# Kernel tuning notes

Measured on AMD Instinct MI355X. Metric: run time of the kernel, lower is better.

The kernel has to match this reference:

```python
import jax, jax.numpy as jnp
import numpy as np

N_NODES = 50000
N_EDGES = 1600000
D_IN = 128
D_E = 64
D_MID = 64
D_CAT = 2 * D_IN + D_E  # 320, input width of first Linear


def setup_inputs() -> dict:
    key = jax.random.key(0)
    ks = jax.random.split(key, 8)
    emb = jax.random.normal(ks[0], (N_NODES, D_IN), dtype=jnp.float32)
    src_idx = jax.random.randint(ks[1], (N_EDGES,), 0, N_NODES, dtype=jnp.int32)
    dst_idx = jax.random.randint(ks[2], (N_EDGES,), 0, N_NODES, dtype=jnp.int32)
    edge_feats = jax.random.normal(ks[3], (N_EDGES, D_E), dtype=jnp.float32)
    # nn.Linear default init: U(-1/sqrt(fan_in), 1/sqrt(fan_in))
    s1 = 1.0 / np.sqrt(D_CAT)
    s2 = 1.0 / np.sqrt(D_MID)
    W1 = jax.random.uniform(ks[4], (D_CAT, D_MID), jnp.float32, -s1, s1)
    b1 = jax.random.uniform(ks[5], (D_MID,), jnp.float32, -s1, s1)
    W2 = jax.random.uniform(ks[6], (D_MID, 1), jnp.float32, -s2, s2)
    b2 = jax.random.uniform(ks[7], (1,), jnp.float32, -s2, s2)
    return {"emb": emb, "src_idx": src_idx, "dst_idx": dst_idx,
            "edge_feats": edge_feats, "W1": W1, "b1": b1, "W2": W2, "b2": b2}


def reference(emb, src_idx, dst_idx, edge_feats, W1, b1, W2, b2):
    # Equivalent to concat([emb[i], emb[j], e_ij]) @ W1, but split so the
    # node-side projections are done once per node, then gathered per edge.
    W1_src = W1[:D_IN]            # [D_IN, D_MID]
    W1_dst = W1[D_IN:2 * D_IN]    # [D_IN, D_MID]
    W1_e = W1[2 * D_IN:]          # [D_E, D_MID]
    proj_src = emb @ W1_src       # [N, D_MID]
    proj_dst = emb @ W1_dst       # [N, D_MID]
    h = proj_src[src_idx] + proj_dst[dst_idx] + edge_feats @ W1_e + b1  # [E, D_MID]
    h = jax.nn.relu(h)
    logits = h @ W2[:, 0] + b2[0]  # [E]
    return logits
```

## Files before the change

kernel.cpp:

```cpp
#include <hip/hip_runtime.h>
#include <hip/hip_bf16.h>
#include <cstddef>

#define D_IN 128
#define D_E 64
#define D_MID 64

typedef __attribute__((ext_vector_type(8))) short bf16x8;
typedef __attribute__((ext_vector_type(4))) float f32x4;
typedef __attribute__((ext_vector_type(4))) int i32x4;

__device__ __forceinline__ short bf16_rne(float f) {
    __hip_bfloat16 h = __float2bfloat16(f);
    union { __hip_bfloat16 h; short s; } u; u.h = h;
    return u.s;
}

__device__ __forceinline__ void split2(float f, short& hi, short& lo) {
    unsigned u  = __float_as_uint(f);
    unsigned uh = u & 0xffff0000u;
    hi = (short)(uh >> 16);
    lo = bf16_rne(f - __uint_as_float(uh));
}

__global__ __launch_bounds__(128) void proj_kernel(
    const float* __restrict__ emb, const float* __restrict__ W1,
    const float* __restrict__ b1, float* __restrict__ P)
{
    const int j  = threadIdx.x;
    const int nb = blockIdx.x * 16;
    const float* Wbase = (j < 64) ? (W1 + j) : (W1 + 128 * 64 + (j - 64));

    float acc[16];
    #pragma unroll
    for (int i = 0; i < 16; ++i) acc[i] = 0.f;

    for (int kc = 0; kc < 8; ++kc) {
        float w[16];
        #pragma unroll
        for (int kk = 0; kk < 16; ++kk) w[kk] = Wbase[(kc * 16 + kk) * 64];
        #pragma unroll
        for (int i = 0; i < 16; ++i) {
            const float* e = emb + (size_t)(nb + i) * 128 + kc * 16;
            #pragma unroll
            for (int kk = 0; kk < 16; ++kk)
                acc[i] = fmaf(e[kk], w[kk], acc[i]);
        }
    }
    const float bias = (j < 64) ? b1[j] : 0.f;
    #pragma unroll
    for (int i = 0; i < 16; ++i)
        P[(size_t)(nb + i) * 128 + j] = acc[i] + bias;
}

__global__ __launch_bounds__(256) void edge_kernel(
    const float* __restrict__ ef,  const int* __restrict__ src,
    const int* __restrict__ dst,   const float* __restrict__ P,
    const float* __restrict__ W1,  const float* __restrict__ W2,
    const float* __restrict__ b2p, float* __restrict__ out)
{
    const int lane = threadIdx.x & 63;
    const int lr   = lane & 15;
    const int lg   = lane >> 4;
    const int wid  = threadIdx.x >> 6;
    const int wave = blockIdx.x * 4 + wid;
    const int ebase0 = wave * 128;

    const float* We = W1 + 256 * 64;
    bf16x8 bhi[2][4], blo[2][4];
    #pragma unroll
    for (int ks = 0; ks < 2; ++ks)
        #pragma unroll
        for (int nt = 0; nt < 4; ++nt) {
            #pragma unroll
            for (int i = 0; i < 8; ++i) {
                int kl = (i < 4) ? (lg * 4 + i) : (16 + lg * 4 + (i - 4));
                float f = We[(ks * 32 + kl) * 64 + nt * 16 + lr];
                short h, l; split2(f, h, l);
                bhi[ks][nt][i] = h; blo[ks][nt][i] = l;
            }
        }

    float w2v[4];
    #pragma unroll
    for (int nt = 0; nt < 4; ++nt) w2v[nt] = W2[nt * 16 + lr];
    const float b2 = b2p[0];

    i32x4 s4 = __builtin_nontemporal_load((const i32x4*)(src + ebase0 + lg * 4));
    i32x4 d4 = __builtin_nontemporal_load((const i32x4*)(dst + ebase0 + lg * 4));

    for (int t = 0; t < 8; ++t) {
        const int eb = ebase0 + t * 16;

        i32x4 s4n, d4n;
        if (t < 7) {
            s4n = __builtin_nontemporal_load((const i32x4*)(src + eb + 16 + lg * 4));
            d4n = __builtin_nontemporal_load((const i32x4*)(dst + eb + 16 + lg * 4));
        }

        f32x4 acc[4];
        #pragma unroll
        for (int nt = 0; nt < 4; ++nt) acc[nt] = (f32x4){0.f, 0.f, 0.f, 0.f};

        #pragma unroll
        for (int ks = 0; ks < 2; ++ks) {
            const float* abase = ef + (size_t)(eb + lr) * 64 + ks * 32 + lg * 4;
            f32x4 a0 = __builtin_nontemporal_load((const f32x4*)(abase));
            f32x4 a1 = __builtin_nontemporal_load((const f32x4*)(abase + 16));
            bf16x8 ahi, alo;
            #pragma unroll
            for (int i = 0; i < 4; ++i) {
                short h, l;
                split2(a0[i], h, l); ahi[i]     = h; alo[i]     = l;
                split2(a1[i], h, l); ahi[i + 4] = h; alo[i + 4] = l;
            }
            #pragma unroll
            for (int nt = 0; nt < 4; ++nt) {
                acc[nt] = __builtin_amdgcn_mfma_f32_16x16x32_bf16(ahi, bhi[ks][nt], acc[nt], 0, 0, 0);
                acc[nt] = __builtin_amdgcn_mfma_f32_16x16x32_bf16(ahi, blo[ks][nt], acc[nt], 0, 0, 0);
                acc[nt] = __builtin_amdgcn_mfma_f32_16x16x32_bf16(alo, bhi[ks][nt], acc[nt], 0, 0, 0);
            }
        }

        #pragma unroll
        for (int r = 0; r < 4; ++r) {
            const float* Ps = P + (size_t)s4[r] * 128 + lr;
            const float* Pd = P + (size_t)d4[r] * 128 + 64 + lr;
            float tot = 0.f;
            #pragma unroll
            for (int nt = 0; nt < 4; ++nt) {
                float h = acc[nt][r] + Ps[nt * 16] + Pd[nt * 16];
                h = fmaxf(h, 0.f);
                tot = fmaf(h, w2v[nt], tot);
            }
            tot += __shfl_xor(tot, 1);
            tot += __shfl_xor(tot, 2);
            tot += __shfl_xor(tot, 4);
            tot += __shfl_xor(tot, 8);
            if (lr == 0)
                __builtin_nontemporal_store(tot + b2, out + eb + lg * 4 + r);
        }

        s4 = s4n; d4 = d4n;
    }
}

extern "C" void kernel_launch(void* const* d_in, const int* in_sizes, int n_in,
                              void* d_out, int out_size, void* d_ws, size_t ws_size,
                              hipStream_t stream) {
    const float* emb = (const float*)d_in[0];
    const int*   src = (const int*)  d_in[1];
    const int*   dst = (const int*)  d_in[2];
    const float* ef  = (const float*)d_in[3];
    const float* W1  = (const float*)d_in[4];
    const float* b1  = (const float*)d_in[5];
    const float* W2  = (const float*)d_in[6];
    const float* b2  = (const float*)d_in[7];
    float* P   = (float*)d_ws;
    float* out = (float*)d_out;

    hipLaunchKernelGGL(proj_kernel, dim3(3125), dim3(128), 0, stream, emb, W1, b1, P);
    hipLaunchKernelGGL(edge_kernel, dim3(3125), dim3(256), 0, stream,
                       ef, src, dst, P, W1, W2, b2, out);
}
```

Before: 744.2 us.

## Issue edge-feature and projection gathers before MFMA, drop weight low-part split

Hoists the edge-feature loads and the P gathers for src/dst to the top of each tile iteration so their latency overlaps the bf16 split and MFMA work. Rounds W1_e to a single bf16 value instead of a hi/lo pair, which cuts one of three MFMAs per tile and halves the weight registers. Adds a launch_bounds occupancy hint of 4 blocks. The cost is lower precision in the edge-weight product and more live registers for the prefetched values.

New measurement: 727.6 us. -2.2%, faster.

```diff
diff --git a/kernel.cpp b/kernel.cpp
--- a/kernel.cpp
+++ b/kernel.cpp
@@ -14,13 +14,6 @@
     __hip_bfloat16 h = __float2bfloat16(f);
     union { __hip_bfloat16 h; short s; } u; u.h = h;
     return u.s;
-}
-
-__device__ __forceinline__ void split2(float f, short& hi, short& lo) {
-    unsigned u  = __float_as_uint(f);
-    unsigned uh = u & 0xffff0000u;
-    hi = (short)(uh >> 16);
-    lo = bf16_rne(f - __uint_as_float(uh));
 }
 
 __global__ __launch_bounds__(128) void proj_kernel(
@@ -53,7 +46,7 @@
         P[(size_t)(nb + i) * 128 + j] = acc[i] + bias;
 }
 
-__global__ __launch_bounds__(256) void edge_kernel(
+__global__ __launch_bounds__(256, 4) void edge_kernel(
     const float* __restrict__ ef,  const int* __restrict__ src,
     const int* __restrict__ dst,   const float* __restrict__ P,
     const float* __restrict__ W1,  const float* __restrict__ W2,
@@ -67,19 +60,16 @@
     const int ebase0 = wave * 128;
 
     const float* We = W1 + 256 * 64;
-    bf16x8 bhi[2][4], blo[2][4];
+    bf16x8 bh[2][4];
     #pragma unroll
     for (int ks = 0; ks < 2; ++ks)
         #pragma unroll
-        for (int nt = 0; nt < 4; ++nt) {
+        for (int nt = 0; nt < 4; ++nt)
             #pragma unroll
             for (int i = 0; i < 8; ++i) {
                 int kl = (i < 4) ? (lg * 4 + i) : (16 + lg * 4 + (i - 4));
-                float f = We[(ks * 32 + kl) * 64 + nt * 16 + lr];
-                short h, l; split2(f, h, l);
-                bhi[ks][nt][i] = h; blo[ks][nt][i] = l;
+                bh[ks][nt][i] = bf16_rne(We[(ks * 32 + kl) * 64 + nt * 16 + lr]);
             }
-        }
 
     float w2v[4];
     #pragma unroll
@@ -91,6 +81,24 @@
 
     for (int t = 0; t < 8; ++t) {
         const int eb = ebase0 + t * 16;
+
+        f32x4 a0[2], a1[2];
+        #pragma unroll
+        for (int ks = 0; ks < 2; ++ks) {
+            const float* ab = ef + (size_t)(eb + lr) * 64 + ks * 32 + lg * 4;
+            a0[ks] = __builtin_nontemporal_load((const f32x4*)(ab));
+            a1[ks] = __builtin_nontemporal_load((const f32x4*)(ab + 16));
+        }
+
+        float padd[4][4];
+        #pragma unroll
+        for (int r = 0; r < 4; ++r) {
+            const float* Ps = P + (size_t)s4[r] * 128 + lr;
+            const float* Pd = P + (size_t)d4[r] * 128 + 64 + lr;
+            #pragma unroll
+            for (int nt = 0; nt < 4; ++nt)
+                padd[r][nt] = Ps[nt * 16] + Pd[nt * 16];
+        }
 
         i32x4 s4n, d4n;
         if (t < 7) {
@@ -104,32 +112,29 @@
 
         #pragma unroll
         for (int ks = 0; ks < 2; ++ks) {
-            const float* abase = ef + (size_t)(eb + lr) * 64 + ks * 32 + lg * 4;
-            f32x4 a0 = __builtin_nontemporal_load((const f32x4*)(abase));
-            f32x4 a1 = __builtin_nontemporal_load((const f32x4*)(abase + 16));
             bf16x8 ahi, alo;
             #pragma unroll
             for (int i = 0; i < 4; ++i) {
-                short h, l;
-                split2(a0[i], h, l); ahi[i]     = h; alo[i]     = l;
-                split2(a1[i], h, l); ahi[i + 4] = h; alo[i + 4] = l;
+                float f0 = a0[ks][i], f1 = a1[ks][i];
+                unsigned u0 = __float_as_uint(f0), u1 = __float_as_uint(f1);
+                ahi[i]     = (short)(u0 >> 16);
+                ahi[i + 4] = (short)(u1 >> 16);
+                alo[i]     = bf16_rne(f0 - __uint_as_float(u0 & 0xffff0000u));
+                alo[i + 4] = bf16_rne(f1 - __uint_as_float(u1 & 0xffff0000u));
             }
             #pragma unroll
             for (int nt = 0; nt < 4; ++nt) {
-                acc[nt] = __builtin_amdgcn_mfma_f32_16x16x32_bf16(ahi, bhi[ks][nt], acc[nt], 0, 0, 0);
-                acc[nt] = __builtin_amdgcn_mfma_f32_16x16x32_bf16(ahi, blo[ks][nt], acc[nt], 0, 0, 0);
-                acc[nt] = __builtin_amdgcn_mfma_f32_16x16x32_bf16(alo, bhi[ks][nt], acc[nt], 0, 0, 0);
+                acc[nt] = __builtin_amdgcn_mfma_f32_16x16x32_bf16(ahi, bh[ks][nt], acc[nt], 0, 0, 0);
+                acc[nt] = __builtin_amdgcn_mfma_f32_16x16x32_bf16(alo, bh[ks][nt], acc[nt], 0, 0, 0);
             }
         }
 
         #pragma unroll
         for (int r = 0; r < 4; ++r) {
-            const float* Ps = P + (size_t)s4[r] * 128 + lr;
-            const float* Pd = P + (size_t)d4[r] * 128 + 64 + lr;
             float tot = 0.f;
             #pragma unroll
             for (int nt = 0; nt < 4; ++nt) {
-                float h = acc[nt][r] + Ps[nt * 16] + Pd[nt * 16];
+                float h = acc[nt][r] + padd[r][nt];
                 h = fmaxf(h, 0.f);
                 tot = fmaf(h, w2v[nt], tot);
             }
```
